# Performance work log

Measured on AMD Instinct MI355X. Metric: run time of the kernel, lower is better.

Reference implementation:

```python
import jax, jax.numpy as jnp
import numpy as np

B, T, DM, H = 4, 2048, 1024, 16
D = DM // H  # head_dim = 64


def setup_inputs() -> dict:
    key = jax.random.key(0)
    ks = jax.random.split(key, 10)
    s = 0.02
    return {
        "query": jax.random.normal(ks[0], (B, T, DM), jnp.float32),
        "key": jax.random.normal(ks[1], (B, T, DM), jnp.float32),
        "value": jax.random.normal(ks[2], (B, T, DM), jnp.float32),
        "Wq": jax.random.normal(ks[3], (DM, DM), jnp.float32) * s,
        "bq": jnp.zeros((DM,), jnp.float32),
        "Wk": jax.random.normal(ks[4], (DM, DM), jnp.float32) * s,
        "bk": jnp.zeros((DM,), jnp.float32),
        "Wv": jax.random.normal(ks[5], (DM, DM), jnp.float32) * s,
        "bv": jnp.zeros((DM,), jnp.float32),
        "Wo": jax.random.normal(ks[6], (DM, DM), jnp.float32) * s,
        "bo": jnp.zeros((DM,), jnp.float32),
        "gate_w": jax.random.normal(ks[7], (H, D, D), jnp.float32) * s,
        "gate_b": jax.random.normal(ks[8], (H, D), jnp.float32),
    }


def _split_heads(x):
    # (B, T, DM) -> (B, H, T, D)
    b, t, _ = x.shape
    return x.reshape(b, t, H, D).transpose(0, 2, 1, 3)


def reference(query, key, value, Wq, bq, Wk, bk, Wv, bv, Wo, bo, gate_w, gate_b):
    q = _split_heads(query @ Wq + bq)   # (B,H,T,D)
    k = _split_heads(key @ Wk + bk)
    v = _split_heads(value @ Wv + bv)
    scale = 1.0 / jnp.sqrt(jnp.asarray(D, q.dtype))
    scores = jnp.einsum("bhqd,bhkd->bhqk", q, k) * scale  # (B,H,Tq,Tk)
    attn = jax.nn.softmax(scores, axis=-1)
    y = jnp.einsum("bhqk,bhkd->bhqd", attn, v)            # (B,H,T,D)
    # per-head elementwise gating: sigmoid(W_h y + b_h)
    gate = jax.nn.sigmoid(jnp.einsum("bhtd,hde->bhte", y, gate_w) + gate_b[None, :, None, :])
    y = y * gate
    y = y.transpose(0, 2, 1, 3).reshape(y.shape[0], y.shape[2], H * D)  # merge heads
    return y @ Wo + bo
```

## Files before the change

kernel.cpp:

```cpp
#include <hip/hip_runtime.h>
#include <stdint.h>

typedef unsigned short u16;
typedef uint32_t u32;
typedef __attribute__((ext_vector_type(8))) short bf16x8;
typedef __attribute__((ext_vector_type(4))) float f32x4;
typedef __attribute__((ext_vector_type(4))) u32 u32x4;

__device__ __forceinline__ u16 f2b(float x) {
  union { float f; uint32_t u; } v; v.f = x;
  uint32_t u = v.u;
  return (u16)((u + 0x7fffu + ((u >> 16) & 1u)) >> 16);
}

__device__ __forceinline__ float fexp2(float x) {
  float r;
  asm("v_exp_f32 %0, %1" : "=v"(r) : "v"(x));
  return r;
}

__device__ __forceinline__ u32 cvtpk(float lo, float hi) {
  u32 r;
  asm("v_cvt_pk_bf16_f32 %0, %1, %2" : "=v"(r) : "v"(lo), "v"(hi));
  return r;
}

__device__ __forceinline__ void gload_lds16(const void* g, void* l) {
  __builtin_amdgcn_global_load_lds(
      (const __attribute__((address_space(1))) void*)g,
      (__attribute__((address_space(3))) void*)l, 16, 0, 0);
}

__global__ __launch_bounds__(256) void cvt3_f32_bf16(const float* __restrict__ q,
                                                     const float* __restrict__ k,
                                                     const float* __restrict__ v,
                                                     u16* __restrict__ xq,
                                                     u16* __restrict__ xk,
                                                     u16* __restrict__ xv, int n4) {
  int idx = blockIdx.x * 256 + threadIdx.x;
  if (idx >= n4) return;
  const int z = blockIdx.y;
  const float* in = z == 0 ? q : z == 1 ? k : v;
  u16* out = z == 0 ? xq : z == 1 ? xk : xv;
  float4 vv = ((const float4*)in)[idx];
  ushort4 o;
  o.x = f2b(vv.x); o.y = f2b(vv.y); o.z = f2b(vv.z); o.w = f2b(vv.w);
  ((ushort4*)out)[idx] = o;
}

__global__ __launch_bounds__(256) void transpose_cvt4(const float* __restrict__ w0,
                                                      const float* __restrict__ w1,
                                                      const float* __restrict__ w2,
                                                      const float* __restrict__ w3,
                                                      u16* __restrict__ o0,
                                                      u16* __restrict__ o1,
                                                      u16* __restrict__ o2,
                                                      u16* __restrict__ o3) {
  __shared__ float t[64][65];
  const int z = blockIdx.z;
  const float* inp = z == 0 ? w0 : z == 1 ? w1 : z == 2 ? w2 : w3;
  u16* outp = z == 0 ? o0 : z == 1 ? o1 : z == 2 ? o2 : o3;
  int r0 = blockIdx.x * 64, c0 = blockIdx.y * 64;
  for (int i = 0; i < 16; ++i) {
    int idx = i * 256 + threadIdx.x;
    int r = idx >> 6, c = idx & 63;
    t[r][c] = inp[(size_t)(r0 + r) * 1024 + (c0 + c)];
  }
  __syncthreads();
  for (int i = 0; i < 16; ++i) {
    int idx = i * 256 + threadIdx.x;
    int c = idx >> 6, r = idx & 63;
    outp[(size_t)(c0 + c) * 1024 + (r0 + r)] = f2b(t[r][c]);
  }
}

__global__ __launch_bounds__(256) void transpose_gate(const float* __restrict__ in,
                                                      u16* __restrict__ out) {
  __shared__ float t[64][65];
  const float* inp = in + (size_t)blockIdx.z * 4096;
  u16* outp = out + (size_t)blockIdx.z * 4096;
  for (int i = 0; i < 16; ++i) {
    int idx = i * 256 + threadIdx.x;
    int r = idx >> 6, c = idx & 63;
    t[r][c] = inp[(size_t)r * 64 + c];
  }
  __syncthreads();
  for (int i = 0; i < 16; ++i) {
    int idx = i * 256 + threadIdx.x;
    int c = idx >> 6, r = idx & 63;
    outp[(size_t)c * 64 + r] = f2b(t[r][c]);
  }
}

template <int MODE>
__device__ __forceinline__ void gemm_body(const u16* __restrict__ A,
                                          const u16* __restrict__ Bt,
                                          const float* __restrict__ bias,
                                          void* __restrict__ Cout,
                                          int M, int N, int K, float scale,
                                          u16* lA, u16* lB, int bm, int bn) {
  const int tid = threadIdx.x;
  const int wave = tid >> 6, lane = tid & 63;
  const int l15 = lane & 15, l4 = lane >> 4;
  const int wr = (wave >> 1) * 64, wc = (wave & 1) * 64;
  f32x4 acc[4][4];
  for (int a = 0; a < 4; ++a)
    for (int b = 0; b < 4; ++b)
      for (int j = 0; j < 4; ++j) acc[a][b][j] = 0.f;
  const u16* Ab = A + (size_t)bm * 128 * K;
  const u16* Bb = Bt + (size_t)bn * 128 * K;
  for (int kt = 0; kt < K; kt += 64) {
    __syncthreads();
#pragma unroll
    for (int i = 0; i < 4; ++i) {
      int p = i * 256 + tid;
      int r = p >> 3, kc = p & 7, skc = kc ^ (r & 7);
      gload_lds16(Ab + (size_t)r * K + kt + skc * 8, &lA[p * 8]);
    }
#pragma unroll
    for (int i = 0; i < 4; ++i) {
      int p = i * 256 + tid;
      int r = p >> 3, kc = p & 7, skc = kc ^ (r & 7);
      gload_lds16(Bb + (size_t)r * K + kt + skc * 8, &lB[p * 8]);
    }
    __syncthreads();
#pragma unroll
    for (int kk = 0; kk < 2; ++kk) {
      const int kch = kk * 4 + l4;
      bf16x8 af[4], bfr[4];
#pragma unroll
      for (int mt = 0; mt < 4; ++mt) {
        int r = wr + mt * 16 + l15;
        af[mt] = *(const bf16x8*)&lA[r * 64 + ((kch ^ (r & 7)) << 3)];
      }
#pragma unroll
      for (int nt = 0; nt < 4; ++nt) {
        int r = wc + nt * 16 + l15;
        bfr[nt] = *(const bf16x8*)&lB[r * 64 + ((kch ^ (r & 7)) << 3)];
      }
      __builtin_amdgcn_s_setprio(1);
#pragma unroll
      for (int mt = 0; mt < 4; ++mt)
#pragma unroll
        for (int nt = 0; nt < 4; ++nt)
          acc[mt][nt] = __builtin_amdgcn_mfma_f32_16x16x32_bf16(af[mt], bfr[nt],
                                                                acc[mt][nt], 0, 0, 0);
      __builtin_amdgcn_s_setprio(0);
    }
  }
  float bval[4];
  float bvalm[4][4];
  if constexpr (MODE == 2) {
#pragma unroll
    for (int mt = 0; mt < 4; ++mt)
#pragma unroll
      for (int i = 0; i < 4; ++i)
        bvalm[mt][i] = bias[bm * 128 + wr + mt * 16 + l4 * 4 + i];
  } else {
#pragma unroll
    for (int nt = 0; nt < 4; ++nt) bval[nt] = bias[bn * 128 + wc + nt * 16 + l15];
  }
#pragma unroll
  for (int mt = 0; mt < 4; ++mt) {
#pragma unroll
    for (int nt = 0; nt < 4; ++nt) {
      int n = bn * 128 + wc + nt * 16 + l15;
#pragma unroll
      for (int i = 0; i < 4; ++i) {
        int m = bm * 128 + wr + mt * 16 + l4 * 4 + i;
        if constexpr (MODE == 0) {
          ((float*)Cout)[(size_t)m * N + n] = acc[mt][nt][i] + bval[nt];
        } else if constexpr (MODE == 1) {
          float v = acc[mt][nt][i] + bval[nt];
          int bb = m >> 11, t = m & 2047, hh = n >> 6, d = n & 63;
          ((u16*)Cout)[(((size_t)bb * 16 + hh) * 2048 + t) * 64 + d] = f2b(v * scale);
        } else {
          float v = acc[mt][nt][i] + bvalm[mt][i];
          int bb = n >> 11, t = n & 2047, hh = m >> 6, d = m & 63;
          ((u16*)Cout)[(((size_t)bb * 16 + hh) * 64 + d) * 2048 + t] = f2b(v);
        }
      }
    }
  }
}

__global__ __launch_bounds__(256) void gemm_qkv(const u16* __restrict__ Xq,
                                                const u16* __restrict__ Xk,
                                                const u16* __restrict__ Xv,
                                                const u16* __restrict__ WqT,
                                                const u16* __restrict__ WkT,
                                                const u16* __restrict__ WvT,
                                                const float* __restrict__ bq,
                                                const float* __restrict__ bk,
                                                const float* __restrict__ bv,
                                                u16* __restrict__ Qb,
                                                u16* __restrict__ Kb,
                                                u16* __restrict__ Vtr, float qscale) {
  __shared__ __align__(16) u16 lA[128 * 64];
  __shared__ __align__(16) u16 lB[128 * 64];
  const int z = blockIdx.z;
  if (z == 2) {
    gemm_body<2>(WvT, Xv, bv, Vtr, 1024, 8192, 1024, 1.0f, lA, lB,
                 blockIdx.y, blockIdx.x);
  } else {
    const u16* A = z == 0 ? Xq : Xk;
    const u16* Bt = z == 0 ? WqT : WkT;
    const float* bias = z == 0 ? bq : bk;
    u16* C = z == 0 ? Qb : Kb;
    float scale = z == 0 ? qscale : 1.0f;
    gemm_body<1>(A, Bt, bias, C, 8192, 1024, 1024, scale, lA, lB,
                 blockIdx.x, blockIdx.y);
  }
}

__global__ __launch_bounds__(256) void gemm_out(const u16* __restrict__ A,
                                                const u16* __restrict__ Bt,
                                                const float* __restrict__ bias,
                                                float* __restrict__ C) {
  __shared__ __align__(16) u16 lA[128 * 64];
  __shared__ __align__(16) u16 lB[128 * 64];
  gemm_body<0>(A, Bt, bias, C, 8192, 1024, 1024, 1.0f, lA, lB,
               blockIdx.x, blockIdx.y);
}

__global__ __launch_bounds__(256) void attn_fused(const u16* __restrict__ Qb,
                                                  const u16* __restrict__ Kb,
                                                  const u16* __restrict__ Vt,
                                                  const u16* __restrict__ GwT,
                                                  const float* __restrict__ gate_b,
                                                  u16* __restrict__ Yg) {
  __shared__ __align__(16) u16 lds[16384];
  const int tid = threadIdx.x;
  const int w = tid >> 6, lane = tid & 63;
  const int l15 = lane & 15, l4 = lane >> 4;
  const int qt = blockIdx.x, bh = blockIdx.y;
  const int b = bh >> 4, h = bh & 15;

  const u16* Qg = Qb + ((size_t)bh * 2048 + qt * 64 + w * 16 + l15) * 64;
  bf16x8 qf0 = *(const bf16x8*)(Qg + l4 * 8);
  bf16x8 qf1 = *(const bf16x8*)(Qg + 32 + l4 * 8);

  const bf16x8 ones = {0x3F80, 0x3F80, 0x3F80, 0x3F80, 0x3F80, 0x3F80, 0x3F80, 0x3F80};
  const f32x4 fz = {0.f, 0.f, 0.f, 0.f};

  f32x4 acc[4];
  f32x4 lsum;
#pragma unroll
  for (int nt = 0; nt < 4; ++nt)
#pragma unroll
    for (int j = 0; j < 4; ++j) acc[nt][j] = 0.f;
#pragma unroll
  for (int j = 0; j < 4; ++j) lsum[j] = 0.f;

  const u16* f0 = lds + l15 * 64 + ((l4 ^ (l15 & 7)) << 3);
  const u16* f1 = lds + l15 * 64 + (((4 + l4) ^ (l15 & 7)) << 3);

  const int r0 = tid >> 3, kc0 = tid & 7, skc = kc0 ^ (r0 & 7);
  const int sr = ((r0 << 1) & 0x38) | ((r0 >> 3) & 4) | (r0 & 3);
  const u16* kp  = Kb + (size_t)bh * 131072 + (size_t)sr * 64 + skc * 8;
  const u16* kp2 = kp + 256;
  const u16* vp  = Vt + (size_t)bh * 131072 + (size_t)r0 * 2048 + skc * 8;
  const u16* vp2 = vp + (size_t)32 * 2048;
  u16* dK = lds + tid * 8;
  u16* dV = lds + 8192 + tid * 8;

#define STAGE(c)                                                     \
  do {                                                               \
    gload_lds16(kp, dK + (c)*4096);                                  \
    gload_lds16(kp2, dK + (c)*4096 + 2048);                          \
    gload_lds16(vp, dV + (c)*4096);                                  \
    gload_lds16(vp2, dV + (c)*4096 + 2048);                          \
    kp += 4096; kp2 += 4096; vp += 64; vp2 += 64;                    \
  } while (0)

#define COMPUTE(c)                                                            \
  do {                                                                        \
    f32x4 s[4];                                                               \
    __builtin_amdgcn_s_setprio(1);                                            \
    _Pragma("unroll") for (int nt = 0; nt < 4; ++nt) {                        \
      bf16x8 kf = *(const bf16x8*)(f0 + (c)*4096 + nt * 1024);                \
      s[nt] = __builtin_amdgcn_mfma_f32_16x16x32_bf16(kf, qf0, fz, 0, 0, 0);  \
    }                                                                         \
    _Pragma("unroll") for (int nt = 0; nt < 4; ++nt) {                        \
      bf16x8 kf = *(const bf16x8*)(f1 + (c)*4096 + nt * 1024);                \
      s[nt] = __builtin_amdgcn_mfma_f32_16x16x32_bf16(kf, qf1, s[nt], 0, 0, 0);\
    }                                                                         \
    __builtin_amdgcn_s_setprio(0);                                           \
    union { u32x4 u; bf16x8 bv; } c0, c1;                                     \
    c0.u[0] = cvtpk(fexp2(s[0][0]), fexp2(s[0][1]));                          \
    c0.u[1] = cvtpk(fexp2(s[0][2]), fexp2(s[0][3]));                          \
    c0.u[2] = cvtpk(fexp2(s[2][0]), fexp2(s[2][1]));                          \
    c0.u[3] = cvtpk(fexp2(s[2][2]), fexp2(s[2][3]));                          \
    c1.u[0] = cvtpk(fexp2(s[1][0]), fexp2(s[1][1]));                          \
    c1.u[1] = cvtpk(fexp2(s[1][2]), fexp2(s[1][3]));                          \
    c1.u[2] = cvtpk(fexp2(s[3][0]), fexp2(s[3][1]));                          \
    c1.u[3] = cvtpk(fexp2(s[3][2]), fexp2(s[3][3]));                          \
    __builtin_amdgcn_s_setprio(1);                                           \
    lsum = __builtin_amdgcn_mfma_f32_16x16x32_bf16(ones, c0.bv, lsum, 0, 0, 0);\
    lsum = __builtin_amdgcn_mfma_f32_16x16x32_bf16(ones, c1.bv, lsum, 0, 0, 0);\
    _Pragma("unroll") for (int nt = 0; nt < 4; ++nt) {                        \
      bf16x8 vf = *(const bf16x8*)(f0 + 8192 + (c)*4096 + nt * 1024);         \
      acc[nt] = __builtin_amdgcn_mfma_f32_16x16x32_bf16(vf, c0.bv, acc[nt], 0, 0, 0);\
    }                                                                         \
    _Pragma("unroll") for (int nt = 0; nt < 4; ++nt) {                        \
      bf16x8 vf = *(const bf16x8*)(f1 + 8192 + (c)*4096 + nt * 1024);         \
      acc[nt] = __builtin_amdgcn_mfma_f32_16x16x32_bf16(vf, c1.bv, acc[nt], 0, 0, 0);\
    }                                                                         \
    __builtin_amdgcn_s_setprio(0);                                           \
  } while (0)

  STAGE(0);
  __syncthreads();
  for (int it = 0; it < 16; ++it) {
    STAGE(1);
    COMPUTE(0);
    __syncthreads();
    if (it < 15) STAGE(0);
    COMPUTE(1);
    __syncthreads();
  }
#undef STAGE
#undef COMPUTE

  float inv = 1.f / lsum[0];
  float y[4][4];
#pragma unroll
  for (int nt = 0; nt < 4; ++nt)
#pragma unroll
    for (int i = 0; i < 4; ++i) y[nt][i] = acc[nt][i] * inv;

  bf16x8 gwf[2][4];
  {
    const u16* g = GwT + (size_t)h * 4096;
#pragma unroll
    for (int kk = 0; kk < 2; ++kk)
#pragma unroll
      for (int et = 0; et < 4; ++et)
        gwf[kk][et] = *(const bf16x8*)(g + (et * 16 + l15) * 64 + (kk * 4 + l4) * 8);
  }

  u32* ws32 = (u32*)lds + w * 1024;
  const int rsw = (l15 & 7) << 2;
#pragma unroll
  for (int nt = 0; nt < 4; ++nt) {
    u32 y0 = cvtpk(y[nt][0], y[nt][1]);
    u32 y1 = cvtpk(y[nt][2], y[nt][3]);
    int col = (nt * 8 + l4 * 2) ^ rsw;
    *(uint64_t*)(ws32 + l15 * 64 + col) = ((uint64_t)y1 << 32) | y0;
  }
  asm volatile("s_waitcnt lgkmcnt(0)" ::: "memory");
  bf16x8 yf[2];
  yf[0] = *(const bf16x8*)(ws32 + l15 * 64 + ((l4 * 4) ^ rsw));
  yf[1] = *(const bf16x8*)(ws32 + l15 * 64 + ((16 + l4 * 4) ^ rsw));

  f32x4 g4[4];
#pragma unroll
  for (int et = 0; et < 4; ++et)
#pragma unroll
    for (int j = 0; j < 4; ++j) g4[et][j] = 0.f;
#pragma unroll
  for (int kk = 0; kk < 2; ++kk)
#pragma unroll
    for (int et = 0; et < 4; ++et)
      g4[et] = __builtin_amdgcn_mfma_f32_16x16x32_bf16(gwf[kk][et], yf[kk], g4[et], 0, 0, 0);

  const float* gb = gate_b + h * 64;
  u32 ok[4][2];
#pragma unroll
  for (int et = 0; et < 4; ++et) {
    float o[4];
#pragma unroll
    for (int i = 0; i < 4; ++i) {
      float gv = g4[et][i] + gb[et * 16 + l4 * 4 + i];
      float sg = 1.f / (1.f + __expf(-gv));
      o[i] = y[et][i] * sg;
    }
    ok[et][0] = cvtpk(o[0], o[1]);
    ok[et][1] = cvtpk(o[2], o[3]);
  }
  asm volatile("s_waitcnt lgkmcnt(0)" ::: "memory");
#pragma unroll
  for (int et = 0; et < 4; ++et) {
    int col = (et * 8 + l4 * 2) ^ rsw;
    *(uint64_t*)(ws32 + l15 * 64 + col) = ((uint64_t)ok[et][1] << 32) | ok[et][0];
  }
  asm volatile("s_waitcnt lgkmcnt(0)" ::: "memory");
  {
    int rr = lane >> 2, c = lane & 3;
    int rs2 = (rr & 7) << 2;
    u32x4 d0 = *(const u32x4*)(ws32 + rr * 64 + ((c * 4) ^ rs2));
    u32x4 d1 = *(const u32x4*)(ws32 + rr * 64 + (((c + 4) * 4) ^ rs2));
    size_t row = (size_t)b * 2048 + qt * 64 + w * 16 + rr;
    u32* og = (u32*)(Yg + row * 1024 + h * 64);
    *(u32x4*)(og + c * 4) = d0;
    *(u32x4*)(og + (c + 4) * 4) = d1;
  }
}

extern "C" void kernel_launch(void* const* d_in, const int* in_sizes, int n_in,
                              void* d_out, int out_size, void* d_ws, size_t ws_size,
                              hipStream_t stream) {
  (void)in_sizes; (void)n_in; (void)out_size; (void)ws_size;
  const float* query  = (const float*)d_in[0];
  const float* key    = (const float*)d_in[1];
  const float* value  = (const float*)d_in[2];
  const float* Wq     = (const float*)d_in[3];
  const float* bq     = (const float*)d_in[4];
  const float* Wk     = (const float*)d_in[5];
  const float* bk     = (const float*)d_in[6];
  const float* Wv     = (const float*)d_in[7];
  const float* bv     = (const float*)d_in[8];
  const float* Wo     = (const float*)d_in[9];
  const float* bo     = (const float*)d_in[10];
  const float* gate_w = (const float*)d_in[11];
  const float* gate_b = (const float*)d_in[12];

  const size_t XN = (size_t)8192 * 1024;
  const size_t WN = (size_t)1024 * 1024;
  char* ws = (char*)d_ws;
  size_t off = 0;
  auto nxt = [&](size_t bytes) {
    char* p = ws + off;
    off += (bytes + 255) & ~(size_t)255;
    return p;
  };
  u16* Xq  = (u16*)nxt(XN * 2);
  u16* Xk  = (u16*)nxt(XN * 2);
  u16* Xv  = (u16*)nxt(XN * 2);
  u16* WqT = (u16*)nxt(WN * 2);
  u16* WkT = (u16*)nxt(WN * 2);
  u16* WvT = (u16*)nxt(WN * 2);
  u16* WoT = (u16*)nxt(WN * 2);
  u16* GwT = (u16*)nxt((size_t)16 * 64 * 64 * 2);
  u16* Qb  = (u16*)nxt(XN * 2);
  u16* Kb  = (u16*)nxt(XN * 2);
  u16* Vtr = (u16*)nxt(XN * 2);
  u16* Yg  = (u16*)nxt(XN * 2);

  int n4 = (int)(XN / 4);
  cvt3_f32_bf16<<<dim3(n4 / 256, 3), 256, 0, stream>>>(query, key, value, Xq, Xk, Xv, n4);
  transpose_cvt4<<<dim3(16, 16, 4), 256, 0, stream>>>(Wq, Wk, Wv, Wo, WqT, WkT, WvT, WoT);
  transpose_gate<<<dim3(1, 1, 16), 256, 0, stream>>>(gate_w, GwT);

  gemm_qkv<<<dim3(64, 8, 3), 256, 0, stream>>>(Xq, Xk, Xv, WqT, WkT, WvT, bq, bk, bv,
                                               Qb, Kb, Vtr, 0.125f * 1.44269504f);
  attn_fused<<<dim3(32, 64), 256, 0, stream>>>(Qb, Kb, Vtr, GwT, gate_b, Yg);
  gemm_out<<<dim3(64, 8), 256, 0, stream>>>(Yg, WoT, bo, (float*)d_out);
}
```

Measured before the change: 222.3 us.

## Process two query tiles per wave in attention to reuse K/V fragments

Each wave now handles 32 query rows (two 16-row groups) instead of 16. Every K and V fragment read from LDS, and every staged K/V tile, therefore feeds twice as many MFMAs. The grid is halved along the query axis and the gating epilogue runs once per group, using separate LDS scratch regions. This cuts LDS read traffic and global K/V loads per query. In exchange it roughly doubles accumulator registers, which can reduce occupancy, and it leaves fewer blocks to spread across CUs.

```diff
diff --git a/kernel.cpp b/kernel.cpp
--- a/kernel.cpp
+++ b/kernel.cpp
@@ -236,21 +236,23 @@
   const int qt = blockIdx.x, bh = blockIdx.y;
   const int b = bh >> 4, h = bh & 15;
 
-  const u16* Qg = Qb + ((size_t)bh * 2048 + qt * 64 + w * 16 + l15) * 64;
-  bf16x8 qf0 = *(const bf16x8*)(Qg + l4 * 8);
-  bf16x8 qf1 = *(const bf16x8*)(Qg + 32 + l4 * 8);
+  const u16* QgA = Qb + ((size_t)bh * 2048 + qt * 128 + w * 32 + l15) * 64;
+  const u16* QgB = QgA + 16 * 64;
+  bf16x8 qA0 = *(const bf16x8*)(QgA + l4 * 8);
+  bf16x8 qA1 = *(const bf16x8*)(QgA + 32 + l4 * 8);
+  bf16x8 qB0 = *(const bf16x8*)(QgB + l4 * 8);
+  bf16x8 qB1 = *(const bf16x8*)(QgB + 32 + l4 * 8);
 
   const bf16x8 ones = {0x3F80, 0x3F80, 0x3F80, 0x3F80, 0x3F80, 0x3F80, 0x3F80, 0x3F80};
   const f32x4 fz = {0.f, 0.f, 0.f, 0.f};
 
-  f32x4 acc[4];
-  f32x4 lsum;
+  f32x4 accA[4], accB[4], lsA, lsB;
 #pragma unroll
   for (int nt = 0; nt < 4; ++nt)
 #pragma unroll
-    for (int j = 0; j < 4; ++j) acc[nt][j] = 0.f;
-#pragma unroll
-  for (int j = 0; j < 4; ++j) lsum[j] = 0.f;
+    for (int j = 0; j < 4; ++j) { accA[nt][j] = 0.f; accB[nt][j] = 0.f; }
+#pragma unroll
+  for (int j = 0; j < 4; ++j) { lsA[j] = 0.f; lsB[j] = 0.f; }
 
   const u16* f0 = lds + l15 * 64 + ((l4 ^ (l15 & 7)) << 3);
   const u16* f1 = lds + l15 * 64 + (((4 + l4) ^ (l15 & 7)) << 3);
@@ -275,38 +277,54 @@
 
 #define COMPUTE(c)                                                            \
   do {                                                                        \
-    f32x4 s[4];                                                               \
+    bf16x8 kf0[4], kf1[4];                                                    \
+    _Pragma("unroll") for (int nt = 0; nt < 4; ++nt) {                        \
+      kf0[nt] = *(const bf16x8*)(f0 + (c)*4096 + nt * 1024);                  \
+      kf1[nt] = *(const bf16x8*)(f1 + (c)*4096 + nt * 1024);                  \
+    }                                                                         \
+    f32x4 sA[4], sB[4];                                                       \
     __builtin_amdgcn_s_setprio(1);                                            \
     _Pragma("unroll") for (int nt = 0; nt < 4; ++nt) {                        \
-      bf16x8 kf = *(const bf16x8*)(f0 + (c)*4096 + nt * 1024);                \
-      s[nt] = __builtin_amdgcn_mfma_f32_16x16x32_bf16(kf, qf0, fz, 0, 0, 0);  \
+      sA[nt] = __builtin_amdgcn_mfma_f32_16x16x32_bf16(kf0[nt], qA0, fz, 0, 0, 0); \
+      sA[nt] = __builtin_amdgcn_mfma_f32_16x16x32_bf16(kf1[nt], qA1, sA[nt], 0, 0, 0); \
+      sB[nt] = __builtin_amdgcn_mfma_f32_16x16x32_bf16(kf0[nt], qB0, fz, 0, 0, 0); \
+      sB[nt] = __builtin_amdgcn_mfma_f32_16x16x32_bf16(kf1[nt], qB1, sB[nt], 0, 0, 0); \
+    }                                                                         \
+    __builtin_amdgcn_s_setprio(0);                                            \
+    union { u32x4 u; bf16x8 bv; } a0, a1, b0, b1;                             \
+    a0.u[0] = cvtpk(fexp2(sA[0][0]), fexp2(sA[0][1]));                        \
+    a0.u[1] = cvtpk(fexp2(sA[0][2]), fexp2(sA[0][3]));                        \
+    a0.u[2] = cvtpk(fexp2(sA[2][0]), fexp2(sA[2][1]));                        \
+    a0.u[3] = cvtpk(fexp2(sA[2][2]), fexp2(sA[2][3]));                        \
+    a1.u[0] = cvtpk(fexp2(sA[1][0]), fexp2(sA[1][1]));                        \
+    a1.u[1] = cvtpk(fexp2(sA[1][2]), fexp2(sA[1][3]));                        \
+    a1.u[2] = cvtpk(fexp2(sA[3][0]), fexp2(sA[3][1]));                        \
+    a1.u[3] = cvtpk(fexp2(sA[3][2]), fexp2(sA[3][3]));                        \
+    b0.u[0] = cvtpk(fexp2(sB[0][0]), fexp2(sB[0][1]));                        \
+    b0.u[1] = cvtpk(fexp2(sB[0][2]), fexp2(sB[0][3]));                        \
+    b0.u[2] = cvtpk(fexp2(sB[2][0]), fexp2(sB[2][1]));                        \
+    b0.u[3] = cvtpk(fexp2(sB[2][2]), fexp2(sB[2][3]));                        \
+    b1.u[0] = cvtpk(fexp2(sB[1][0]), fexp2(sB[1][1]));                        \
+    b1.u[1] = cvtpk(fexp2(sB[1][2]), fexp2(sB[1][3]));                        \
+    b1.u[2] = cvtpk(fexp2(sB[3][0]), fexp2(sB[3][1]));                        \
+    b1.u[3] = cvtpk(fexp2(sB[3][2]), fexp2(sB[3][3]));                        \
+    __builtin_amdgcn_s_setprio(1);                                            \
+    lsA = __builtin_amdgcn_mfma_f32_16x16x32_bf16(ones, a0.bv, lsA, 0, 0, 0); \
+    lsA = __builtin_amdgcn_mfma_f32_16x16x32_bf16(ones, a1.bv, lsA, 0, 0, 0); \
+    lsB = __builtin_amdgcn_mfma_f32_16x16x32_bf16(ones, b0.bv, lsB, 0, 0, 0); \
+    lsB = __builtin_amdgcn_mfma_f32_16x16x32_bf16(ones, b1.bv, lsB, 0, 0, 0); \
+    bf16x8 vf0[4], vf1[4];                                                    \
+    _Pragma("unroll") for (int nt = 0; nt < 4; ++nt) {                        \
+      vf0[nt] = *(const bf16x8*)(f0 + 8192 + (c)*4096 + nt * 1024);           \
+      vf1[nt] = *(const bf16x8*)(f1 + 8192 + (c)*4096 + nt * 1024);           \
     }                                                                         \
     _Pragma("unroll") for (int nt = 0; nt < 4; ++nt) {                        \
-      bf16x8 kf = *(const bf16x8*)(f1 + (c)*4096 + nt * 1024);                \
-      s[nt] = __builtin_amdgcn_mfma_f32_16x16x32_bf16(kf, qf1, s[nt], 0, 0, 0);\
+      accA[nt] = __builtin_amdgcn_mfma_f32_16x16x32_bf16(vf0[nt], a0.bv, accA[nt], 0, 0, 0); \
+      accA[nt] = __builtin_amdgcn_mfma_f32_16x16x32_bf16(vf1[nt], a1.bv, accA[nt], 0, 0, 0); \
+      accB[nt] = __builtin_amdgcn_mfma_f32_16x16x32_bf16(vf0[nt], b0.bv, accB[nt], 0, 0, 0); \
+      accB[nt] = __builtin_amdgcn_mfma_f32_16x16x32_bf16(vf1[nt], b1.bv, accB[nt], 0, 0, 0); \
     }                                                                         \
-    __builtin_amdgcn_s_setprio(0);                                           \
-    union { u32x4 u; bf16x8 bv; } c0, c1;                                     \
-    c0.u[0] = cvtpk(fexp2(s[0][0]), fexp2(s[0][1]));                          \
-    c0.u[1] = cvtpk(fexp2(s[0][2]), fexp2(s[0][3]));                          \
-    c0.u[2] = cvtpk(fexp2(s[2][0]), fexp2(s[2][1]));                          \
-    c0.u[3] = cvtpk(fexp2(s[2][2]), fexp2(s[2][3]));                          \
-    c1.u[0] = cvtpk(fexp2(s[1][0]), fexp2(s[1][1]));                          \
-    c1.u[1] = cvtpk(fexp2(s[1][2]), fexp2(s[1][3]));                          \
-    c1.u[2] = cvtpk(fexp2(s[3][0]), fexp2(s[3][1]));                          \
-    c1.u[3] = cvtpk(fexp2(s[3][2]), fexp2(s[3][3]));                          \
-    __builtin_amdgcn_s_setprio(1);                                           \
-    lsum = __builtin_amdgcn_mfma_f32_16x16x32_bf16(ones, c0.bv, lsum, 0, 0, 0);\
-    lsum = __builtin_amdgcn_mfma_f32_16x16x32_bf16(ones, c1.bv, lsum, 0, 0, 0);\
-    _Pragma("unroll") for (int nt = 0; nt < 4; ++nt) {                        \
-      bf16x8 vf = *(const bf16x8*)(f0 + 8192 + (c)*4096 + nt * 1024);         \
-      acc[nt] = __builtin_amdgcn_mfma_f32_16x16x32_bf16(vf, c0.bv, acc[nt], 0, 0, 0);\
-    }                                                                         \
-    _Pragma("unroll") for (int nt = 0; nt < 4; ++nt) {                        \
-      bf16x8 vf = *(const bf16x8*)(f1 + 8192 + (c)*4096 + nt * 1024);         \
-      acc[nt] = __builtin_amdgcn_mfma_f32_16x16x32_bf16(vf, c1.bv, acc[nt], 0, 0, 0);\
-    }                                                                         \
-    __builtin_amdgcn_s_setprio(0);                                           \
+    __builtin_amdgcn_s_setprio(0);                                            \
   } while (0)
 
   STAGE(0);
@@ -322,13 +340,6 @@
 #undef STAGE
 #undef COMPUTE
 
-  float inv = 1.f / lsum[0];
-  float y[4][4];
-#pragma unroll
-  for (int nt = 0; nt < 4; ++nt)
-#pragma unroll
-    for (int i = 0; i < 4; ++i) y[nt][i] = acc[nt][i] * inv;
-
   bf16x8 gwf[2][4];
   {
     const u16* g = GwT + (size_t)h * 4096;
@@ -338,63 +349,64 @@
       for (int et = 0; et < 4; ++et)
         gwf[kk][et] = *(const bf16x8*)(g + (et * 16 + l15) * 64 + (kk * 4 + l4) * 8);
   }
-
-  u32* ws32 = (u32*)lds + w * 1024;
+  const float* gb = gate_b + h * 64;
   const int rsw = (l15 & 7) << 2;
-#pragma unroll
-  for (int nt = 0; nt < 4; ++nt) {
-    u32 y0 = cvtpk(y[nt][0], y[nt][1]);
-    u32 y1 = cvtpk(y[nt][2], y[nt][3]);
-    int col = (nt * 8 + l4 * 2) ^ rsw;
-    *(uint64_t*)(ws32 + l15 * 64 + col) = ((uint64_t)y1 << 32) | y0;
-  }
-  asm volatile("s_waitcnt lgkmcnt(0)" ::: "memory");
-  bf16x8 yf[2];
-  yf[0] = *(const bf16x8*)(ws32 + l15 * 64 + ((l4 * 4) ^ rsw));
-  yf[1] = *(const bf16x8*)(ws32 + l15 * 64 + ((16 + l4 * 4) ^ rsw));
-
-  f32x4 g4[4];
-#pragma unroll
-  for (int et = 0; et < 4; ++et)
-#pragma unroll
-    for (int j = 0; j < 4; ++j) g4[et][j] = 0.f;
-#pragma unroll
-  for (int kk = 0; kk < 2; ++kk)
-#pragma unroll
-    for (int et = 0; et < 4; ++et)
-      g4[et] = __builtin_amdgcn_mfma_f32_16x16x32_bf16(gwf[kk][et], yf[kk], g4[et], 0, 0, 0);
-
-  const float* gb = gate_b + h * 64;
-  u32 ok[4][2];
-#pragma unroll
-  for (int et = 0; et < 4; ++et) {
-    float o[4];
-#pragma unroll
-    for (int i = 0; i < 4; ++i) {
-      float gv = g4[et][i] + gb[et * 16 + l4 * 4 + i];
-      float sg = 1.f / (1.f + __expf(-gv));
-      o[i] = y[et][i] * sg;
-    }
-    ok[et][0] = cvtpk(o[0], o[1]);
-    ok[et][1] = cvtpk(o[2], o[3]);
-  }
-  asm volatile("s_waitcnt lgkmcnt(0)" ::: "memory");
-#pragma unroll
-  for (int et = 0; et < 4; ++et) {
-    int col = (et * 8 + l4 * 2) ^ rsw;
-    *(uint64_t*)(ws32 + l15 * 64 + col) = ((uint64_t)ok[et][1] << 32) | ok[et][0];
-  }
-  asm volatile("s_waitcnt lgkmcnt(0)" ::: "memory");
-  {
-    int rr = lane >> 2, c = lane & 3;
-    int rs2 = (rr & 7) << 2;
-    u32x4 d0 = *(const u32x4*)(ws32 + rr * 64 + ((c * 4) ^ rs2));
-    u32x4 d1 = *(const u32x4*)(ws32 + rr * 64 + (((c + 4) * 4) ^ rs2));
-    size_t row = (size_t)b * 2048 + qt * 64 + w * 16 + rr;
-    u32* og = (u32*)(Yg + row * 1024 + h * 64);
-    *(u32x4*)(og + c * 4) = d0;
-    *(u32x4*)(og + (c + 4) * 4) = d1;
-  }
+
+#define EPILOGUE(accX, lsX, g)                                                 \
+  do {                                                                         \
+    float inv = 1.f / lsX[0];                                                  \
+    float y[4][4];                                                             \
+    _Pragma("unroll") for (int nt = 0; nt < 4; ++nt)                           \
+      _Pragma("unroll") for (int i = 0; i < 4; ++i) y[nt][i] = accX[nt][i] * inv; \
+    u32* ws32 = (u32*)lds + w * 2048 + (g)*1024;                               \
+    _Pragma("unroll") for (int nt = 0; nt < 4; ++nt) {                         \
+      u32 y0 = cvtpk(y[nt][0], y[nt][1]);                                      \
+      u32 y1 = cvtpk(y[nt][2], y[nt][3]);                                      \
+      int col = (nt * 8 + l4 * 2) ^ rsw;                                       \
+      *(uint64_t*)(ws32 + l15 * 64 + col) = ((uint64_t)y1 << 32) | y0;         \
+    }                                                                          \
+    asm volatile("s_waitcnt lgkmcnt(0)" ::: "memory");                         \
+    bf16x8 yf[2];                                                              \
+    yf[0] = *(const bf16x8*)(ws32 + l15 * 64 + ((l4 * 4) ^ rsw));              \
+    yf[1] = *(const bf16x8*)(ws32 + l15 * 64 + ((16 + l4 * 4) ^ rsw));         \
+    f32x4 g4[4];                                                               \
+    _Pragma("unroll") for (int et = 0; et < 4; ++et)                           \
+      _Pragma("unroll") for (int j = 0; j < 4; ++j) g4[et][j] = 0.f;           \
+    _Pragma("unroll") for (int kk = 0; kk < 2; ++kk)                           \
+      _Pragma("unroll") for (int et = 0; et < 4; ++et)                         \
+        g4[et] = __builtin_amdgcn_mfma_f32_16x16x32_bf16(gwf[kk][et], yf[kk], g4[et], 0, 0, 0); \
+    u32 ok[4][2];                                                              \
+    _Pragma("unroll") for (int et = 0; et < 4; ++et) {                         \
+      float o[4];                                                              \
+      _Pragma("unroll") for (int i = 0; i < 4; ++i) {                          \
+        float gv = g4[et][i] + gb[et * 16 + l4 * 4 + i];                       \
+        float sg = 1.f / (1.f + __expf(-gv));                                  \
+        o[i] = y[et][i] * sg;                                                  \
+      }                                                                        \
+      ok[et][0] = cvtpk(o[0], o[1]);                                           \
+      ok[et][1] = cvtpk(o[2], o[3]);                                           \
+    }                                                                          \
+    asm volatile("s_waitcnt lgkmcnt(0)" ::: "memory");                         \
+    _Pragma("unroll") for (int et = 0; et < 4; ++et) {                         \
+      int col = (et * 8 + l4 * 2) ^ rsw;                                       \
+      *(uint64_t*)(ws32 + l15 * 64 + col) = ((uint64_t)ok[et][1] << 32) | ok[et][0]; \
+    }                                                                          \
+    asm volatile("s_waitcnt lgkmcnt(0)" ::: "memory");                         \
+    {                                                                          \
+      int rr = lane >> 2, c = lane & 3;                                        \
+      int rs2 = (rr & 7) << 2;                                                 \
+      u32x4 d0 = *(const u32x4*)(ws32 + rr * 64 + ((c * 4) ^ rs2));            \
+      u32x4 d1 = *(const u32x4*)(ws32 + rr * 64 + (((c + 4) * 4) ^ rs2));      \
+      size_t row = (size_t)b * 2048 + qt * 128 + w * 32 + (g)*16 + rr;         \
+      u32* og = (u32*)(Yg + row * 1024 + h * 64);                              \
+      *(u32x4*)(og + c * 4) = d0;                                              \
+      *(u32x4*)(og + (c + 4) * 4) = d1;                                        \
+    }                                                                          \
+  } while (0)
+
+  EPILOGUE(accA, lsA, 0);
+  EPILOGUE(accB, lsB, 1);
+#undef EPILOGUE
 }
 
 extern "C" void kernel_launch(void* const* d_in, const int* in_sizes, int n_in,
@@ -444,6 +456,6 @@
 
   gemm_qkv<<<dim3(64, 8, 3), 256, 0, stream>>>(Xq, Xk, Xv, WqT, WkT, WvT, bq, bk, bv,
                                                Qb, Kb, Vtr, 0.125f * 1.44269504f);
-  attn_fused<<<dim3(32, 64), 256, 0, stream>>>(Qb, Kb, Vtr, GwT, gate_b, Yg);
+  attn_fused<<<dim3(16, 64), 256, 0, stream>>>(Qb, Kb, Vtr, GwT, gate_b, Yg);
   gemm_out<<<dim3(64, 8), 256, 0, stream>>>(Yg, WoT, bo, (float*)d_out);
 }
```

Result: faster. 209.6 us (-5.7%).
